# Performance work log

Measured on AMD Instinct MI355X. Metric: run time of the kernel, lower is better.

The kernel has to match this reference:

```python
import jax, jax.numpy as jnp
import numpy as np

D_MODEL = 1024
NUM_HEADS = 16
D_K = D_MODEL // NUM_HEADS
SCALE = 1.0 / (D_K ** 0.5)


def setup_inputs() -> dict:
    key = jax.random.key(0)
    k1, k2, k3 = jax.random.split(key, 3)
    x = jax.random.normal(k1, (2, 2048, D_MODEL), dtype=jnp.float32)
    # torch nn.Linear weight layout: [out_features, in_features]; y = x @ W.T
    w_qkv = jax.random.normal(k2, (3 * D_MODEL, D_MODEL), dtype=jnp.float32) * (1.0 / np.sqrt(D_MODEL))
    w_out = jax.random.normal(k3, (D_MODEL, D_MODEL), dtype=jnp.float32) * (1.0 / np.sqrt(D_MODEL))
    return {"x": x, "w_qkv": w_qkv, "w_out": w_out}


def reference(x, w_qkv, w_out):
    b, s, _ = x.shape
    qkv = jnp.einsum("bsd,ed->bse", x, w_qkv)            # [b, s, 3*d_model]
    q, k, v = jnp.split(qkv, 3, axis=-1)
    # [b, s, h, d_k] -> [b, h, s, d_k]
    q = q.reshape(b, s, NUM_HEADS, D_K).transpose(0, 2, 1, 3)
    k = k.reshape(b, s, NUM_HEADS, D_K).transpose(0, 2, 1, 3)
    v = v.reshape(b, s, NUM_HEADS, D_K).transpose(0, 2, 1, 3)
    scores = jnp.einsum("bhqd,bhkd->bhqk", q, k) * SCALE   # [b, h, s, s]
    attn = jax.nn.softmax(scores, axis=-1)
    ctx = jnp.einsum("bhqk,bhkd->bhqd", attn, v)           # [b, h, s, d_k]
    ctx = ctx.transpose(0, 2, 1, 3).reshape(b, s, D_MODEL)
    return jnp.einsum("bsd,ed->bse", ctx, w_out)
```

## Files before the change

### kernel.cpp

```cpp
#include <hip/hip_runtime.h>

typedef __attribute__((ext_vector_type(8))) short bf16x8;
typedef __attribute__((ext_vector_type(4))) float f32x4;
typedef __attribute__((ext_vector_type(16))) float f32x16;
typedef __attribute__((ext_vector_type(4))) unsigned int u32x4;

#define MFMA16(A, B, C) __builtin_amdgcn_mfma_f32_16x16x32_bf16((A), (B), (C), 0, 0, 0)
#define MFMA32(A, B, C) __builtin_amdgcn_mfma_f32_32x32x16_bf16((A), (B), (C), 0, 0, 0)

static __device__ __forceinline__ unsigned short f32_to_bf16(float f) {
    unsigned int u = __builtin_bit_cast(unsigned int, f);
    u += 0x7fffu + ((u >> 16) & 1u);
    return (unsigned short)(u >> 16);
}

static __device__ __forceinline__ unsigned int cvtpk(float lo, float hi) {
    unsigned int r;
    asm("v_cvt_pk_bf16_f32 %0, %1, %2" : "=v"(r) : "v"(lo), "v"(hi));
    return r;
}

static __device__ __forceinline__ void gload16(const unsigned short* g, unsigned short* l) {
    __builtin_amdgcn_global_load_lds(
        (const __attribute__((address_space(1))) unsigned int*)g,
        (__attribute__((address_space(3))) unsigned int*)l, 16, 0, 0);
}

#define QSCALE 0.18033688011112042f

__global__ void cast3_f32_bf16(const float* __restrict__ x, const float* __restrict__ wq,
                               const float* __restrict__ wo,
                               unsigned short* __restrict__ xb, unsigned short* __restrict__ wqb,
                               unsigned short* __restrict__ wob) {
    int i = blockIdx.x * 256 + threadIdx.x;
    const float* src;
    unsigned short* dst;
    int off;
    if (i < 1048576)      { src = x;  dst = xb;  off = i; }
    else if (i < 1835008) { src = wq; dst = wqb; off = i - 1048576; }
    else                  { src = wo; dst = wob; off = i - 1835008; }
    float4 v = reinterpret_cast<const float4*>(src)[off];
    ushort4 o;
    o.x = f32_to_bf16(v.x);
    o.y = f32_to_bf16(v.y);
    o.z = f32_to_bf16(v.z);
    o.w = f32_to_bf16(v.w);
    reinterpret_cast<ushort4*>(dst)[off] = o;
}

template <int MODE, int BM, int BN, int WR, int WC>
__global__ __launch_bounds__(256, 2)
void gemm_bt(const unsigned short* __restrict__ Ag,
             const unsigned short* __restrict__ Bg,
             int N, int K,
             unsigned short* __restrict__ qO,
             unsigned short* __restrict__ kO,
             unsigned short* __restrict__ vO,
             float* __restrict__ fO)
{
    constexpr int BK = 64;
    constexpr int MFR = BM / WR / 16;
    constexpr int NFR = BN / WC / 16;
    __shared__ unsigned short sA[BM * BK];
    __shared__ unsigned short sB[BN * BK];

    const int m0 = blockIdx.y * BM;
    const int n0 = blockIdx.x * BN;
    const int t = threadIdx.x;
    const int lane = t & 63;
    const int wid = t >> 6;
    const int wr = wid / WC, wc = wid % WC;
    const int g = lane >> 4, r = lane & 15;
    const int lr8 = lane >> 3, lc = lane & 7;

    const f32x4 fzero = {0.f, 0.f, 0.f, 0.f};
    f32x4 acc[MFR][NFR];
#pragma unroll
    for (int mi = 0; mi < MFR; ++mi)
#pragma unroll
        for (int ni = 0; ni < NFR; ++ni) acc[mi][ni] = fzero;

    for (int k0 = 0; k0 < K; k0 += BK) {
        __syncthreads();
#pragma unroll
        for (int rep = 0; rep < BM / 32; ++rep) {
            const int rbase = rep * 32 + wid * 8;
            const int row = rbase + lr8;
            const int cs = lc ^ (row & 7);
            gload16(&Ag[(size_t)(m0 + row) * K + k0 + cs * 8], &sA[rbase * 64]);
        }
#pragma unroll
        for (int rep = 0; rep < BN / 32; ++rep) {
            const int rbase = rep * 32 + wid * 8;
            const int row = rbase + lr8;
            const int cs = lc ^ (row & 7);
            gload16(&Bg[(size_t)(n0 + row) * K + k0 + cs * 8], &sB[rbase * 64]);
        }
        __syncthreads();

#pragma unroll
        for (int ks = 0; ks < BK; ks += 32) {
            const int c = (ks >> 3) + g;
            bf16x8 af[MFR], bfr[NFR];
#pragma unroll
            for (int mi = 0; mi < MFR; ++mi) {
                const int row = wr * (BM / WR) + mi * 16 + r;
                af[mi] = *reinterpret_cast<const bf16x8*>(&sA[row * BK + ((c * 8) ^ ((row & 7) * 8))]);
            }
#pragma unroll
            for (int ni = 0; ni < NFR; ++ni) {
                const int row = wc * (BN / WC) + ni * 16 + r;
                bfr[ni] = *reinterpret_cast<const bf16x8*>(&sB[row * BK + ((c * 8) ^ ((row & 7) * 8))]);
            }
#pragma unroll
            for (int mi = 0; mi < MFR; ++mi)
#pragma unroll
                for (int ni = 0; ni < NFR; ++ni)
                    acc[mi][ni] = MFMA16(af[mi], bfr[ni], acc[mi][ni]);
        }
    }

#pragma unroll
    for (int mi = 0; mi < MFR; ++mi) {
#pragma unroll
        for (int ni = 0; ni < NFR; ++ni) {
            const int mbase = m0 + wr * (BM / WR) + mi * 16 + 4 * g;
            const int n = n0 + wc * (BN / WC) + ni * 16 + r;
            if (MODE == 0) {
                const int b = mbase >> 11, s = mbase & 2047;
                const int which = n >> 10;
                const int h = (n >> 6) & 15;
                const int d = n & 63;
                if (which == 2) {
                    ushort4 v4;
                    v4.x = f32_to_bf16(acc[mi][ni][0]);
                    v4.y = f32_to_bf16(acc[mi][ni][1]);
                    v4.z = f32_to_bf16(acc[mi][ni][2]);
                    v4.w = f32_to_bf16(acc[mi][ni][3]);
                    *reinterpret_cast<ushort4*>(&vO[(((size_t)(b * 16 + h)) * 64 + d) * 2048 + s]) = v4;
                } else {
                    const size_t dst = (((size_t)(b * 16 + h)) * 2048 + s) * 64 + d;
#pragma unroll
                    for (int i = 0; i < 4; ++i) {
                        const float val = acc[mi][ni][i];
                        if (which == 0) qO[dst + (size_t)i * 64] = f32_to_bf16(val * QSCALE);
                        else            kO[dst + (size_t)i * 64] = f32_to_bf16(val);
                    }
                }
            } else {
#pragma unroll
                for (int i = 0; i < 4; ++i)
                    fO[(size_t)(mbase + i) * N + n] = acc[mi][ni][i];
            }
        }
    }
}

__global__ __launch_bounds__(512, 4)
void attn_kernel(const unsigned short* __restrict__ Q,
                 const unsigned short* __restrict__ Kg,
                 const unsigned short* __restrict__ Vtg,
                 unsigned short* __restrict__ ctx)
{
    const int S = 2048;
    const int bid = blockIdx.x;
    const int swz = (bid & 7) * 64 + (bid >> 3);
    const int hb = swz >> 4;
    const int qb = swz & 15;
    const unsigned short* Qh = Q + (size_t)hb * S * 64;
    const unsigned short* Kh = Kg + (size_t)hb * S * 64;
    const unsigned short* Vh = Vtg + (size_t)hb * 64 * S;

    const int t = threadIdx.x, lane = t & 63, wid = t >> 6;
    const int half = wid >> 2, wq = wid & 3;
    const int l31 = lane & 31, lhi = lane >> 5;
    const int lr8 = lane >> 3, lc = lane & 7;
    const int q0 = qb * 128 + wq * 32;
    const int kbase = half * 1024;

    const int krow = (l31 & 19) | ((l31 & 4) << 1) | ((l31 & 8) >> 1);
    const int ksw = (krow & 7) ^ ((krow >> 3) & 3);
    const int vsw = (l31 & 7) ^ ((l31 >> 3) & 3);

    __shared__ unsigned short smem[2][2][2][64 * 64];

    bf16x8 qf[4];
#pragma unroll
    for (int dstep = 0; dstep < 4; ++dstep)
        qf[dstep] = *reinterpret_cast<const bf16x8*>(
            &Qh[(size_t)(q0 + l31) * 64 + dstep * 16 + lhi * 8]);

    f32x16 acc[2];
#pragma unroll
    for (int dt = 0; dt < 2; ++dt)
#pragma unroll
        for (int i = 0; i < 16; ++i) acc[dt][i] = 0.f;
    float lrun = 0.f;

#define STAGE(buf, k0)                                                                       \
    {                                                                                        \
        _Pragma("unroll")                                                                    \
        for (int rep = 0; rep < 2; ++rep) {                                                  \
            const int rbase = wq * 16 + rep * 8;                                             \
            const int row = rbase + lr8;                                                     \
            const int cs = lc ^ ((row & 7) ^ ((row >> 3) & 3));                              \
            gload16(&Kh[(size_t)((k0) + row) * 64 + cs * 8], &smem[half][buf][0][rbase * 64]); \
            gload16(&Vh[(size_t)row * S + (k0) + cs * 8], &smem[half][buf][1][rbase * 64]);  \
        }                                                                                    \
    }

    STAGE(0, kbase);

    for (int it = 0; it < 16; ++it) {
        __syncthreads();
        const int cur = it & 1;
        if (it < 15) {
            const int kn = kbase + (it + 1) * 64;
            if (cur) STAGE(0, kn) else STAGE(1, kn);
        }
        const unsigned short* kb = smem[half][cur][0];
        const unsigned short* vb = smem[half][cur][1];

        f32x16 st0, st1;
#pragma unroll
        for (int i = 0; i < 16; ++i) { st0[i] = 0.f; st1[i] = 0.f; }
        __builtin_amdgcn_s_setprio(1);
#pragma unroll
        for (int dstep = 0; dstep < 4; ++dstep) {
            const int c = dstep * 2 + lhi;
            bf16x8 kf0 = *reinterpret_cast<const bf16x8*>(&kb[krow * 64 + ((c ^ ksw) * 8)]);
            bf16x8 kf1 = *reinterpret_cast<const bf16x8*>(&kb[(32 + krow) * 64 + ((c ^ ksw) * 8)]);
            st0 = MFMA32(kf0, qf[dstep], st0);
            st1 = MFMA32(kf1, qf[dstep], st1);
        }
        __builtin_amdgcn_s_setprio(0);

#pragma unroll
        for (int i = 0; i < 16; ++i) {
            st0[i] = __builtin_amdgcn_exp2f(st0[i]);
            st1[i] = __builtin_amdgcn_exp2f(st1[i]);
        }
        float s8[8];
#pragma unroll
        for (int j = 0; j < 8; ++j)
            s8[j] = (st0[j] + st0[j + 8]) + (st1[j] + st1[j + 8]);
        lrun += ((s8[0] + s8[1]) + (s8[2] + s8[3])) + ((s8[4] + s8[5]) + (s8[6] + s8[7]));

        bf16x8 pf[4];
#define PACK8(stv, base, out)                                                  \
        {                                                                      \
            u32x4 wv;                                                          \
            wv[0] = cvtpk(stv[(base) + 0], stv[(base) + 1]);                   \
            wv[1] = cvtpk(stv[(base) + 2], stv[(base) + 3]);                   \
            wv[2] = cvtpk(stv[(base) + 4], stv[(base) + 5]);                   \
            wv[3] = cvtpk(stv[(base) + 6], stv[(base) + 7]);                   \
            out = __builtin_bit_cast(bf16x8, wv);                              \
        }
        PACK8(st0, 0, pf[0])
        PACK8(st0, 8, pf[1])
        PACK8(st1, 0, pf[2])
        PACK8(st1, 8, pf[3])
#undef PACK8

        __builtin_amdgcn_s_setprio(1);
#pragma unroll
        for (int dt = 0; dt < 2; ++dt) {
            const int rowd = dt * 32 + l31;
#pragma unroll
            for (int ks = 0; ks < 4; ++ks) {
                const int c = ks * 2 + lhi;
                bf16x8 vf = *reinterpret_cast<const bf16x8*>(&vb[rowd * 64 + ((c ^ vsw) * 8)]);
                acc[dt] = MFMA32(vf, pf[ks], acc[dt]);
            }
        }
        __builtin_amdgcn_s_setprio(0);
    }
#undef STAGE

    lrun += __shfl_xor(lrun, 32);

    __syncthreads();
    float* cb = reinterpret_cast<float*>(&smem[0][0][0][0]);
    if (half == 1) {
        float* base = cb + wq * 2112;
#pragma unroll
        for (int dt = 0; dt < 2; ++dt)
#pragma unroll
            for (int i = 0; i < 16; ++i)
                base[(dt * 16 + i) * 64 + lane] = acc[dt][i];
        if (lhi == 0) base[2048 + l31] = lrun;
    }
    __syncthreads();
    if (half == 0) {
        float* base = cb + wq * 2112;
        const float l1 = base[2048 + l31];
        const float rl = __builtin_amdgcn_rcpf(lrun + l1);
        const int b = hb >> 4, hh = hb & 15;
        const size_t rowbase = ((size_t)(b * 2048 + q0 + l31)) * 1024 + hh * 64;
#pragma unroll
        for (int dt = 0; dt < 2; ++dt) {
#pragma unroll
            for (int rg = 0; rg < 4; ++rg) {
                float v0 = (acc[dt][4 * rg + 0] + base[(dt * 16 + 4 * rg + 0) * 64 + lane]) * rl;
                float v1 = (acc[dt][4 * rg + 1] + base[(dt * 16 + 4 * rg + 1) * 64 + lane]) * rl;
                float v2 = (acc[dt][4 * rg + 2] + base[(dt * 16 + 4 * rg + 2) * 64 + lane]) * rl;
                float v3 = (acc[dt][4 * rg + 3] + base[(dt * 16 + 4 * rg + 3) * 64 + lane]) * rl;
                uint2 o;
                o.x = cvtpk(v0, v1);
                o.y = cvtpk(v2, v3);
                const int dbase = dt * 32 + rg * 8 + lhi * 4;
                *reinterpret_cast<uint2*>(&ctx[rowbase + dbase]) = o;
            }
        }
    }
}

extern "C" void kernel_launch(void* const* d_in, const int* in_sizes, int n_in,
                              void* d_out, int out_size, void* d_ws, size_t ws_size,
                              hipStream_t stream) {
    const float* x     = (const float*)d_in[0];
    const float* w_qkv = (const float*)d_in[1];
    const float* w_out = (const float*)d_in[2];
    float* out = (float*)d_out;

    unsigned short* xb    = (unsigned short*)d_ws;
    unsigned short* wqkvb = xb + 4194304;
    unsigned short* woutb = wqkvb + 3145728;
    unsigned short* qB    = woutb + 1048576;
    unsigned short* kB    = qB + 4194304;
    unsigned short* vB    = kB + 4194304;
    unsigned short* ctxB  = vB + 4194304;

    cast3_f32_bf16<<<8192, 256, 0, stream>>>(x, w_qkv, w_out, xb, wqkvb, woutb);

    gemm_bt<0, 128, 128, 2, 2><<<dim3(24, 32), 256, 0, stream>>>(xb, wqkvb, 3072, 1024, qB, kB, vB, nullptr);

    attn_kernel<<<512, 512, 0, stream>>>(qB, kB, vB, ctxB);

    gemm_bt<1, 64, 128, 1, 4><<<dim3(8, 64), 256, 0, stream>>>(ctxB, woutb, 1024, 1024, nullptr, nullptr, nullptr, out);
}
```

Baseline: 103.0 us.

## Software-pipeline attention loop: overlap next QK MFMA with current softmax/PV

Restructures the attention inner loop into 32-key half-steps with a 4-slot K ring buffer and 2-slot V buffers. The QK^T MFMA for the next step is issued before the exp2/pack/PV work of the current step, using ping-pong score registers. Explicit vmcnt waits with raw s_barrier replace __syncthreads. The aim is to hide MFMA latency behind the softmax VALU work and overlap loads better, at the cost of more registers and tighter synchronisation that must stay correct.

```diff
diff --git a/kernel.cpp b/kernel.cpp
--- a/kernel.cpp
+++ b/kernel.cpp
@@ -182,7 +182,9 @@
     const int ksw = (krow & 7) ^ ((krow >> 3) & 3);
     const int vsw = (l31 & 7) ^ ((l31 >> 3) & 3);
 
-    __shared__ unsigned short smem[2][2][2][64 * 64];
+    __shared__ unsigned short smem[32768];
+#define SKBASE(h, s) (&smem[(h) * 8192 + (s) * 2048])
+#define SVBASE(h, s) (&smem[16384 + (h) * 8192 + (s) * 4096])
 
     bf16x8 qf[4];
 #pragma unroll
@@ -197,90 +199,99 @@
         for (int i = 0; i < 16; ++i) acc[dt][i] = 0.f;
     float lrun = 0.f;
 
-#define STAGE(buf, k0)                                                                       \
-    {                                                                                        \
-        _Pragma("unroll")                                                                    \
-        for (int rep = 0; rep < 2; ++rep) {                                                  \
-            const int rbase = wq * 16 + rep * 8;                                             \
-            const int row = rbase + lr8;                                                     \
-            const int cs = lc ^ ((row & 7) ^ ((row >> 3) & 3));                              \
-            gload16(&Kh[(size_t)((k0) + row) * 64 + cs * 8], &smem[half][buf][0][rbase * 64]); \
-            gload16(&Vh[(size_t)row * S + (k0) + cs * 8], &smem[half][buf][1][rbase * 64]);  \
-        }                                                                                    \
-    }
-
-    STAGE(0, kbase);
-
-    for (int it = 0; it < 16; ++it) {
-        __syncthreads();
-        const int cur = it & 1;
-        if (it < 15) {
-            const int kn = kbase + (it + 1) * 64;
-            if (cur) STAGE(0, kn) else STAGE(1, kn);
-        }
-        const unsigned short* kb = smem[half][cur][0];
-        const unsigned short* vb = smem[half][cur][1];
-
-        f32x16 st0, st1;
-#pragma unroll
-        for (int i = 0; i < 16; ++i) { st0[i] = 0.f; st1[i] = 0.f; }
-        __builtin_amdgcn_s_setprio(1);
-#pragma unroll
-        for (int dstep = 0; dstep < 4; ++dstep) {
-            const int c = dstep * 2 + lhi;
-            bf16x8 kf0 = *reinterpret_cast<const bf16x8*>(&kb[krow * 64 + ((c ^ ksw) * 8)]);
-            bf16x8 kf1 = *reinterpret_cast<const bf16x8*>(&kb[(32 + krow) * 64 + ((c ^ ksw) * 8)]);
-            st0 = MFMA32(kf0, qf[dstep], st0);
-            st1 = MFMA32(kf1, qf[dstep], st1);
-        }
-        __builtin_amdgcn_s_setprio(0);
-
-#pragma unroll
-        for (int i = 0; i < 16; ++i) {
-            st0[i] = __builtin_amdgcn_exp2f(st0[i]);
-            st1[i] = __builtin_amdgcn_exp2f(st1[i]);
-        }
-        float s8[8];
-#pragma unroll
-        for (int j = 0; j < 8; ++j)
-            s8[j] = (st0[j] + st0[j + 8]) + (st1[j] + st1[j + 8]);
-        lrun += ((s8[0] + s8[1]) + (s8[2] + s8[3])) + ((s8[4] + s8[5]) + (s8[6] + s8[7]));
-
-        bf16x8 pf[4];
-#define PACK8(stv, base, out)                                                  \
-        {                                                                      \
-            u32x4 wv;                                                          \
-            wv[0] = cvtpk(stv[(base) + 0], stv[(base) + 1]);                   \
-            wv[1] = cvtpk(stv[(base) + 2], stv[(base) + 3]);                   \
-            wv[2] = cvtpk(stv[(base) + 4], stv[(base) + 5]);                   \
-            wv[3] = cvtpk(stv[(base) + 6], stv[(base) + 7]);                   \
-            out = __builtin_bit_cast(bf16x8, wv);                              \
-        }
-        PACK8(st0, 0, pf[0])
-        PACK8(st0, 8, pf[1])
-        PACK8(st1, 0, pf[2])
-        PACK8(st1, 8, pf[3])
-#undef PACK8
-
-        __builtin_amdgcn_s_setprio(1);
-#pragma unroll
-        for (int dt = 0; dt < 2; ++dt) {
-            const int rowd = dt * 32 + l31;
-#pragma unroll
-            for (int ks = 0; ks < 4; ++ks) {
-                const int c = ks * 2 + lhi;
-                bf16x8 vf = *reinterpret_cast<const bf16x8*>(&vb[rowd * 64 + ((c ^ vsw) * 8)]);
-                acc[dt] = MFMA32(vf, pf[ks], acc[dt]);
-            }
-        }
-        __builtin_amdgcn_s_setprio(0);
-    }
-#undef STAGE
+#define STAGE_K(slot, k0)                                                                  \
+    {                                                                                      \
+        const int rbase_ = wq * 8;                                                         \
+        const int row_ = rbase_ + lr8;                                                     \
+        const int cs_ = lc ^ ((row_ & 7) ^ ((row_ >> 3) & 3));                             \
+        gload16(&Kh[(size_t)((k0) + row_) * 64 + cs_ * 8], SKBASE(half, slot) + rbase_ * 64); \
+    }
+#define STAGE_V(slot, rep, k0)                                                             \
+    {                                                                                      \
+        const int rbase_ = wq * 16 + (rep) * 8;                                            \
+        const int row_ = rbase_ + lr8;                                                     \
+        const int cs_ = lc ^ ((row_ & 7) ^ ((row_ >> 3) & 3));                             \
+        gload16(&Vh[(size_t)row_ * S + (k0) + cs_ * 8], SVBASE(half, slot) + rbase_ * 64); \
+    }
+#define QKSTEP(slot, OUT)                                                                  \
+    {                                                                                      \
+        _Pragma("unroll")                                                                  \
+        for (int i_ = 0; i_ < 16; ++i_) OUT[i_] = 0.f;                                     \
+        const unsigned short* kb_ = SKBASE(half, slot);                                    \
+        __builtin_amdgcn_s_setprio(1);                                                     \
+        _Pragma("unroll")                                                                  \
+        for (int ds_ = 0; ds_ < 4; ++ds_) {                                                \
+            const int c_ = ds_ * 2 + lhi;                                                  \
+            bf16x8 kf_ = *reinterpret_cast<const bf16x8*>(&kb_[krow * 64 + ((c_ ^ ksw) * 8)]); \
+            OUT = MFMA32(kf_, qf[ds_], OUT);                                               \
+        }                                                                                  \
+        __builtin_amdgcn_s_setprio(0);                                                     \
+    }
+#define BODY(T, IN, OUT)                                                                   \
+    {                                                                                      \
+        if ((T) < 30) STAGE_K(((T) + 2) & 3, kbase + ((T) + 2) * 32);                      \
+        if ((T) < 30) asm volatile("s_waitcnt vmcnt(1)" ::: "memory");                     \
+        else          asm volatile("s_waitcnt vmcnt(0)" ::: "memory");                     \
+        __builtin_amdgcn_s_barrier();                                                      \
+        if ((T) < 30) STAGE_V((((T) >> 1) + 1) & 1, (T) & 1, kbase + (((T) >> 1) + 1) * 64); \
+        if ((T) < 31) QKSTEP(((T) + 1) & 3, OUT);                                          \
+        _Pragma("unroll")                                                                  \
+        for (int i_ = 0; i_ < 16; ++i_) IN[i_] = __builtin_amdgcn_exp2f(IN[i_]);           \
+        {                                                                                  \
+            float s8_[8];                                                                  \
+            _Pragma("unroll")                                                              \
+            for (int j_ = 0; j_ < 8; ++j_) s8_[j_] = IN[j_] + IN[j_ + 8];                  \
+            lrun += ((s8_[0] + s8_[1]) + (s8_[2] + s8_[3])) +                              \
+                    ((s8_[4] + s8_[5]) + (s8_[6] + s8_[7]));                               \
+        }                                                                                  \
+        {                                                                                  \
+            bf16x8 pf_[2];                                                                 \
+            u32x4 w0_, w1_;                                                                \
+            w0_[0] = cvtpk(IN[0], IN[1]);  w0_[1] = cvtpk(IN[2], IN[3]);                   \
+            w0_[2] = cvtpk(IN[4], IN[5]);  w0_[3] = cvtpk(IN[6], IN[7]);                   \
+            w1_[0] = cvtpk(IN[8], IN[9]);  w1_[1] = cvtpk(IN[10], IN[11]);                 \
+            w1_[2] = cvtpk(IN[12], IN[13]); w1_[3] = cvtpk(IN[14], IN[15]);                \
+            pf_[0] = __builtin_bit_cast(bf16x8, w0_);                                      \
+            pf_[1] = __builtin_bit_cast(bf16x8, w1_);                                      \
+            const unsigned short* vb_ = SVBASE(half, ((T) >> 1) & 1);                      \
+            __builtin_amdgcn_s_setprio(1);                                                 \
+            _Pragma("unroll")                                                              \
+            for (int dt_ = 0; dt_ < 2; ++dt_) {                                            \
+                const int rowd_ = dt_ * 32 + l31;                                          \
+                _Pragma("unroll")                                                          \
+                for (int ks_ = 0; ks_ < 2; ++ks_) {                                        \
+                    const int c_ = ((T) & 1) * 4 + ks_ * 2 + lhi;                          \
+                    bf16x8 vf_ = *reinterpret_cast<const bf16x8*>(                         \
+                        &vb_[rowd_ * 64 + ((c_ ^ vsw) * 8)]);                              \
+                    acc[dt_] = MFMA32(vf_, pf_[ks_], acc[dt_]);                            \
+                }                                                                          \
+            }                                                                              \
+            __builtin_amdgcn_s_setprio(0);                                                 \
+        }                                                                                  \
+    }
+
+    STAGE_K(0, kbase);
+    STAGE_K(1, kbase + 32);
+    STAGE_V(0, 0, kbase);
+    STAGE_V(0, 1, kbase);
+    asm volatile("s_waitcnt vmcnt(0)" ::: "memory");
+    __builtin_amdgcn_s_barrier();
+    f32x16 stA, stB;
+    QKSTEP(0, stA);
+
+    for (int tt = 0; tt < 32; tt += 2) {
+        BODY(tt, stA, stB)
+        BODY(tt + 1, stB, stA)
+    }
+#undef BODY
+#undef QKSTEP
+#undef STAGE_V
+#undef STAGE_K
 
     lrun += __shfl_xor(lrun, 32);
 
     __syncthreads();
-    float* cb = reinterpret_cast<float*>(&smem[0][0][0][0]);
+    float* cb = reinterpret_cast<float*>(&smem[0]);
     if (half == 1) {
         float* base = cb + wq * 2112;
 #pragma unroll
@@ -313,6 +324,8 @@
             }
         }
     }
+#undef SKBASE
+#undef SVBASE
 }
 
 extern "C" void kernel_launch(void* const* d_in, const int* in_sizes, int n_in,
```

Measured after the change: 117.1 us. 13.6% more time.
